# Kernel optimization log

Hardware: AMD Instinct MI355X
Metric: run time of the kernel (lower is better)

The kernel has to match this reference:

```python
import jax, jax.numpy as jnp
import numpy as np


def _rms(x, w=None, eps=1e-6):
    # RMSNorm in fp32 like the torch module, optional elementwise affine.
    x32 = x.astype(jnp.float32)
    r = jax.lax.rsqrt(jnp.mean(x32 * x32, axis=-1, keepdims=True) + eps)
    y = (x32 * r).astype(x.dtype)
    return y * w if w is not None else y


def _rotate_half(x):
    x1, x2 = jnp.split(x, 2, axis=-1)
    return jnp.concatenate([-x2, x1], axis=-1)


def setup_inputs() -> dict:
    key = jax.random.key(0)
    ks = jax.random.split(key, 10)
    B, N, C, H = 16, 1024, 1152, 16
    hd = C // H          # 72
    hid = 3072           # _swiglu_hidden(1152, 4.0)
    grid = 32            # grid**2 == N
    quarter = hd // 4    # 18
    # exact axial RoPE cache (build_axial_rope_cache)
    inv_freq = 1.0 / (10000.0 ** (np.arange(quarter, dtype=np.float32) / quarter))
    pos = np.arange(grid, dtype=np.float32)
    f1 = pos[:, None] * inv_freq[None, :]                               # (grid, quarter)
    fy = np.broadcast_to(f1[:, None, :], (grid, grid, quarter)).reshape(-1, quarter)
    fx = np.broadcast_to(f1[None, :, :], (grid, grid, quarter)).reshape(-1, quarter)

    def cs(f):
        e = np.concatenate([f, f], axis=-1)                             # (N, hd//2)
        return jnp.asarray(np.cos(e))[None, None], jnp.asarray(np.sin(e))[None, None]

    cos_y, sin_y = cs(fy)
    cos_x, sin_x = cs(fx)

    def w(k, shp, scale=0.02):
        return jax.random.normal(k, shp, jnp.float32) * scale

    return {
        "x": jax.random.normal(ks[0], (B, N, C), jnp.float32),
        "temb": jax.random.normal(ks[1], (B, C), jnp.float32),
        "cos_y": cos_y, "sin_y": sin_y, "cos_x": cos_x, "sin_x": sin_x,
        "Wqkv": w(ks[2], (3 * C, C)), "bqkv": jnp.zeros((3 * C,), jnp.float32),
        "Wt": w(ks[3], (3 * C, C)), "bt": jnp.zeros((3 * C,), jnp.float32),
        "Wp": w(ks[4], (C, C)), "bp": jnp.zeros((C,), jnp.float32),
        "qn_w": jnp.ones((hd,), jnp.float32), "kn_w": jnp.ones((hd,), jnp.float32),
        "Wg": w(ks[5], (hid, C)), "bg": jnp.zeros((hid,), jnp.float32),
        "Wu": w(ks[6], (hid, C)), "bu": jnp.zeros((hid,), jnp.float32),
        "Wd": w(ks[7], (C, hid)), "bd": jnp.zeros((C,), jnp.float32),
    }


def reference(x, temb, cos_y, sin_y, cos_x, sin_x, Wqkv, bqkv, Wt, bt, Wp, bp,
              qn_w, kn_w, Wg, bg, Wu, bu, Wd, bd):
    B, N, C = x.shape
    H = 16
    hd = C // H

    # --- TMSA attention branch ---
    xn = _rms(x)                                            # norm1 (no affine)
    qkv = xn @ Wqkv.T + bqkv + (temb @ Wt.T + bt)[:, None, :]
    qkv = qkv.reshape(B, N, 3, H, hd).transpose(2, 0, 3, 1, 4)  # (3,B,H,N,hd)
    q, k, v = qkv[0], qkv[1], qkv[2]
    q = _rms(q, qn_w)
    k = _rms(k, kn_w)

    def rope(t):
        ty, tx = jnp.split(t, 2, axis=-1)
        ty = ty * cos_y + _rotate_half(ty) * sin_y
        tx = tx * cos_x + _rotate_half(tx) * sin_x
        return jnp.concatenate([ty, tx], axis=-1)

    q, k = rope(q), rope(k)

    scores = jnp.einsum('bhnd,bhmd->bhnm', q, k) / jnp.sqrt(jnp.float32(hd))
    attn = jax.nn.softmax(scores, axis=-1)
    o = jnp.einsum('bhnm,bhmd->bhnd', attn, v)
    o = o.transpose(0, 2, 1, 3).reshape(B, N, C)
    x = x + (o @ Wp.T + bp)

    # --- SwiGLU MLP branch ---
    xn2 = _rms(x)                                           # norm2 (no affine)
    h = jax.nn.silu(xn2 @ Wg.T + bg) * (xn2 @ Wu.T + bu)
    x = x + (h @ Wd.T + bd)
    return x
```

## Files before the change

kernel.cpp:

```cpp
#include <hip/hip_runtime.h>
#include <cstdint>
#include <cstddef>

typedef unsigned short u16;
typedef unsigned int u32;
typedef __attribute__((ext_vector_type(8))) short bf16x8s;
typedef __attribute__((ext_vector_type(4))) float f32x4;

__device__ __forceinline__ u16 f2bf(float f){
  union { float f; unsigned u; } v; v.f = f;
  unsigned r = v.u + 0x7FFFu + ((v.u >> 16) & 1u);
  return (u16)(r >> 16);
}
__device__ __forceinline__ float bf2f(u16 h){
  union { unsigned u; float f; } v; v.u = ((unsigned)h) << 16;
  return v.f;
}

__global__ __launch_bounds__(256) void cvt_kernel(const float* __restrict__ in,
                                                  u16* __restrict__ out, int n){
  int i = blockIdx.x*256 + threadIdx.x;
  if (i < n) out[i] = f2bf(in[i]);
}

__global__ __launch_bounds__(256) void cvt_gu_kernel(const float* __restrict__ Wg,
                                                     const float* __restrict__ Wu,
                                                     u16* __restrict__ out){
  size_t i = (size_t)blockIdx.x*256 + threadIdx.x;
  if (i >= (size_t)6144*1152) return;
  int j = (int)(i / 1152), k = (int)(i % 1152);
  int b16 = j >> 4, w = j & 15;
  int src = (b16 >> 1)*16 + w;
  const float* W = (b16 & 1) ? Wu : Wg;
  out[i] = f2bf(W[(size_t)src*1152 + k]);
}

__global__ __launch_bounds__(256) void temb_kernel(const float* __restrict__ temb,
                                                   const float* __restrict__ Wt,
                                                   const float* __restrict__ bt,
                                                   const float* __restrict__ bqkv,
                                                   float* __restrict__ tvec){
  const int col  = blockIdx.x*4 + (threadIdx.x>>6);
  const int lane = threadIdx.x & 63;
  const float* wp = Wt + (size_t)col*1152;
  float w[18];
  #pragma unroll
  for (int j=0;j<18;j++) w[j] = wp[lane + j*64];
  float acc[16];
  #pragma unroll
  for (int b=0;b<16;b++) acc[b] = 0.f;
  #pragma unroll
  for (int j=0;j<18;j++){
    const int k = lane + j*64;
    #pragma unroll
    for (int b=0;b<16;b++) acc[b] += w[j]*temb[b*1152 + k];
  }
  #pragma unroll
  for (int b=0;b<16;b++){
    #pragma unroll
    for (int d=1; d<64; d<<=1) acc[b] += __shfl_xor(acc[b], d);
  }
  if (lane == 0){
    float add = bt[col] + bqkv[col];
    #pragma unroll
    for (int b=0;b<16;b++) tvec[(size_t)b*3456 + col] = acc[b] + add;
  }
}

__global__ __launch_bounds__(256) void rms_kernel(const float* __restrict__ in,
                                                  u16* __restrict__ out, int C){
  int row = blockIdx.x;
  const float* p = in + (size_t)row*C;
  float ss = 0.f;
  for (int c = threadIdx.x; c < C; c += 256){ float v = p[c]; ss += v*v; }
  #pragma unroll
  for (int d=1; d<64; d<<=1) ss += __shfl_xor(ss, d);
  __shared__ float wsum[4];
  if ((threadIdx.x & 63) == 0) wsum[threadIdx.x>>6] = ss;
  __syncthreads();
  float tot = wsum[0]+wsum[1]+wsum[2]+wsum[3];
  float r = rsqrtf(tot/(float)C + 1e-6f);
  u16* o = out + (size_t)row*C;
  for (int c = threadIdx.x; c < C; c += 256) o[c] = f2bf(p[c]*r);
}

template<int MODE>
__global__ __launch_bounds__(512, 4) void gemm_kernel(
    const u16* __restrict__ A, const u16* __restrict__ B,
    int M, int N, int K, int nbx, int segw,
    const float* __restrict__ bias, const float* __restrict__ fextra,
    void* __restrict__ outv, u16* __restrict__ out2, u16* __restrict__ out3)
{
  __shared__ __align__(16) u16 As0[256*32];
  __shared__ __align__(16) u16 As1[256*32];
  __shared__ __align__(16) u16 As2[256*32];
  __shared__ __align__(16) u16 Bs0[128*32];
  __shared__ __align__(16) u16 Bs1[128*32];
  __shared__ __align__(16) u16 Bs2[128*32];
  const int tid  = threadIdx.x;
  const int lane = tid & 63;
  const int wv   = tid >> 6;
  const int wr   = wv >> 1, wc = wv & 1;

  const int nwg  = (int)gridDim.x;
  const int bid  = (int)blockIdx.x;
  const int xcd  = bid & 7;
  const int slot = bid >> 3;
  const int mdep = (nwg >> 3) / nbx;
  const int segsz = mdep * segw;
  const int seg  = slot / segsz;
  const int rem  = slot - seg*segsz;
  const int mi   = rem / segw;
  const int ni   = seg*segw + (rem - mi*segw);
  const long m0 = (long)(xcd*mdep + mi) * 256;
  const long n0 = (long)ni * 128;

  const u16* Ab = A + (size_t)m0*K;
  const u16* Bb = B + (size_t)n0*K;

  const int gsw  = ((lane&3) ^ ((lane>>3)&3)) * 8;
  const int srow = lane >> 2;

  f32x4 acc[4][4];
  #pragma unroll
  for (int i=0;i<4;i++)
    #pragma unroll
    for (int j=0;j<4;j++) acc[i][j] = (f32x4){0.f,0.f,0.f,0.f};

  auto stage = [&](u16* as, u16* bs, int kt){
    __builtin_amdgcn_global_load_lds(
      (const __attribute__((address_space(1))) void*)(Ab + (size_t)(wv*16 + srow)*K + kt + gsw),
      (__attribute__((address_space(3))) void*)(as + wv*512), 16, 0, 0);
    __builtin_amdgcn_global_load_lds(
      (const __attribute__((address_space(1))) void*)(Ab + (size_t)(128 + wv*16 + srow)*K + kt + gsw),
      (__attribute__((address_space(3))) void*)(as + 4096 + wv*512), 16, 0, 0);
    __builtin_amdgcn_global_load_lds(
      (const __attribute__((address_space(1))) void*)(Bb + (size_t)(wv*16 + srow)*K + kt + gsw),
      (__attribute__((address_space(3))) void*)(bs + wv*512), 16, 0, 0);
  };
  auto compute = [&](const u16* as, const u16* bs){
    const int swc = (((lane>>4) ^ ((lane>>1)&3))) * 8;
    const int lc16 = lane & 15;
    bf16x8s af[4], bfr[4];
    #pragma unroll
    for (int i=0;i<4;i++)
      af[i] = *(const bf16x8s*)(as + (wr*64 + i*16 + lc16)*32 + swc);
    #pragma unroll
    for (int j=0;j<4;j++)
      bfr[j] = *(const bf16x8s*)(bs + (wc*64 + j*16 + lc16)*32 + swc);
    #pragma unroll
    for (int i=0;i<4;i++)
      #pragma unroll
      for (int j=0;j<4;j++)
        acc[i][j] = __builtin_amdgcn_mfma_f32_16x16x32_bf16(af[i], bfr[j], acc[i][j], 0,0,0);
  };

  const int NT = K >> 5;
  stage(As0, Bs0, 0);
  stage(As1, Bs1, 32);
  asm volatile("s_waitcnt vmcnt(3)" ::: "memory");
  __builtin_amdgcn_s_barrier();
  __builtin_amdgcn_sched_barrier(0);

  for (int t = 0; t < NT; t += 3){
    if (t+2 < NT) stage(As2, Bs2, (t+2)*32);
    compute(As0, Bs0);
    if (t+2 < NT) asm volatile("s_waitcnt vmcnt(3)" ::: "memory");
    else          asm volatile("s_waitcnt vmcnt(0)" ::: "memory");
    __builtin_amdgcn_s_barrier();
    __builtin_amdgcn_sched_barrier(0);
    if (t+3 < NT) stage(As0, Bs0, (t+3)*32);
    compute(As1, Bs1);
    if (t+3 < NT) asm volatile("s_waitcnt vmcnt(3)" ::: "memory");
    else          asm volatile("s_waitcnt vmcnt(0)" ::: "memory");
    __builtin_amdgcn_s_barrier();
    __builtin_amdgcn_sched_barrier(0);
    if (t+4 < NT) stage(As1, Bs1, (t+4)*32);
    compute(As2, Bs2);
    if (t+4 < NT) asm volatile("s_waitcnt vmcnt(3)" ::: "memory");
    else          asm volatile("s_waitcnt vmcnt(0)" ::: "memory");
    __builtin_amdgcn_s_barrier();
    __builtin_amdgcn_sched_barrier(0);
  }

  const int lr = (lane>>4)*4, lc = lane&15;
  if (MODE==5){
    #pragma unroll
    for (int i=0;i<4;i++){
      #pragma unroll
      for (int jp=0;jp<2;jp++){
        long hcol = (n0>>1) + wc*32 + jp*16 + lc;
        float bgv = bias[hcol], buv = fextra[hcol];
        #pragma unroll
        for (int r=0;r<4;r++){
          long rowg = m0 + wr*64 + i*16 + lr + r;
          float gv = acc[i][2*jp][r] + bgv;
          float uv = acc[i][2*jp+1][r] + buv;
          float hv = (gv/(1.f + __expf(-gv))) * uv;
          ((u16*)outv)[(size_t)rowg*3072 + hcol] = f2bf(hv);
        }
      }
    }
    return;
  }
  #pragma unroll
  for (int i=0;i<4;i++){
    #pragma unroll
    for (int j=0;j<4;j++){
      long colg = n0 + wc*64 + j*16 + lc;
      long rowg0 = m0 + wr*64 + i*16 + lr;
      if (MODE==0){
        int cg = (int)colg;
        int which = cg / 1152;
        int rem2 = cg - which*1152;
        int hh = rem2 / 72, dd = rem2 - hh*72;
        int b = (int)(rowg0 >> 10), n = (int)(rowg0 & 1023);
        size_t bh = (size_t)(b*16 + hh);
        float tadd = fextra[(size_t)b*3456 + colg];
        if (which == 2){
          ushort4 vv;
          vv.x = f2bf(acc[i][j][0] + tadd);
          vv.y = f2bf(acc[i][j][1] + tadd);
          vv.z = f2bf(acc[i][j][2] + tadd);
          vv.w = f2bf(acc[i][j][3] + tadd);
          *(ushort4*)(out3 + (bh*72 + dd)*1024 + n) = vv;
        } else {
          u16* dst = (which==0) ? (u16*)outv : out2;
          #pragma unroll
          for (int r=0;r<4;r++)
            dst[(bh*1024 + (size_t)(n + r))*72 + dd] = f2bf(acc[i][j][r] + tadd);
        }
      } else {
        #pragma unroll
        for (int r=0;r<4;r++){
          long rowg = rowg0 + r;
          float v = acc[i][j][r];
          size_t oi = (size_t)rowg*N + colg;
          v += bias[colg] + fextra[oi];
          ((float*)outv)[oi] = v;
        }
      }
    }
  }
}

__global__ __launch_bounds__(256) void qkrope_kernel(
    u16* __restrict__ Q, u16* __restrict__ K,
    const float* __restrict__ qn_w, const float* __restrict__ kn_w,
    const float* __restrict__ cos_y, const float* __restrict__ sin_y,
    const float* __restrict__ cos_x, const float* __restrict__ sin_x)
{
  const int gw   = blockIdx.x*4 + (threadIdx.x>>6);
  const int lane = threadIdx.x & 63;
  const int n = gw & 1023;
  const int d0 = lane*2;
  const bool act = d0 < 72;
  const float scale = 0.11785113019775793f;

  u16* qp = Q + (size_t)gw*72;
  u16* kp = K + (size_t)gw*72;
  float q0=0,q1=0,k0=0,k1=0,wq0=0,wq1=0,wk0=0,wk1=0;
  if (act){
    q0 = bf2f(qp[d0]); q1 = bf2f(qp[d0+1]);
    k0 = bf2f(kp[d0]); k1 = bf2f(kp[d0+1]);
    wq0 = qn_w[d0]; wq1 = qn_w[d0+1];
    wk0 = kn_w[d0]; wk1 = kn_w[d0+1];
  }
  float ssq = q0*q0 + q1*q1;
  float ssk = k0*k0 + k1*k1;
  #pragma unroll
  for (int d=1; d<64; d<<=1){ ssq += __shfl_xor(ssq,d); ssk += __shfl_xor(ssk,d); }
  const float rq = rsqrtf(ssq*(1.f/72.f) + 1e-6f);
  const float rk = rsqrtf(ssk*(1.f/72.f) + 1e-6f);
  float qn0 = q0*rq*wq0, qn1 = q1*rq*wq1;
  float kn0 = k0*rk*wk0, kn1 = k1*rk*wk1;

  int dh = d0 % 36;
  const bool first = (dh < 18);
  int partner = first ? lane+9 : lane-9;
  if (!act) partner = lane;
  float pq0 = __shfl(qn0, partner), pq1 = __shfl(qn1, partner);
  float pk0 = __shfl(kn0, partner), pk1 = __shfl(kn1, partner);
  if (act){
    const float* cp = (d0 < 36) ? cos_y : cos_x;
    const float* sp = (d0 < 36) ? sin_y : sin_x;
    float c0 = cp[n*36+dh], c1 = cp[n*36+dh+1];
    float s0 = sp[n*36+dh], s1 = sp[n*36+dh+1];
    float sgn = first ? -1.f : 1.f;
    float qo0 = (qn0*c0 + sgn*pq0*s0)*scale, qo1 = (qn1*c1 + sgn*pq1*s1)*scale;
    float ko0 = kn0*c0 + sgn*pk0*s0,         ko1 = kn1*c1 + sgn*pk1*s1;
    *(unsigned*)(qp + d0) = (unsigned)f2bf(qo0) | ((unsigned)f2bf(qo1)<<16);
    *(unsigned*)(kp + d0) = (unsigned)f2bf(ko0) | ((unsigned)f2bf(ko1)<<16);
  }
}

__global__ __launch_bounds__(256, 3) void attn_kernel(
    const u16* __restrict__ Q, const u16* __restrict__ K,
    const u16* __restrict__ Vt, u16* __restrict__ O)
{
  const int tid  = threadIdx.x;
  const int lane = tid & 63;
  const int wv   = tid >> 6;
  const int g = lane >> 4, c = lane & 15;
  const int bid  = blockIdx.x;
  const int head = (bid >> 6) * 8 + (bid & 7);
  const int q0   = ((bid >> 3) & 7) * 128;
  const int b = head >> 4, h = head & 15;

  __shared__ __align__(16) u16 Vlds[80][72];
  __shared__ __align__(16) u16 Plds[8][16][64];

  const bf16x8s zf = {0,0,0,0,0,0,0,0};
  const u16* Kp = K + (size_t)head*1024*72;
  const u16* Qb = Q + ((size_t)head*1024 + q0 + wv*32)*72;
  const char* Vg = (const char*)(Vt + (size_t)head*72*1024);

  bf16x8s qf[2][3];
  #pragma unroll
  for (int s=0;s<2;s++){
    const u16* qrow = Qb + (size_t)(s*16 + c)*72;
    qf[s][0] = *(const bf16x8s*)(qrow + g*8);
    qf[s][1] = *(const bf16x8s*)(qrow + 32 + g*8);
    qf[s][2] = (g==0) ? *(const bf16x8s*)(qrow + 64) : zf;
  }

  f32x4 oacc[2][5];
  float lsum[2] = {0.f, 0.f};
  #pragma unroll
  for (int s=0;s<2;s++)
    #pragma unroll
    for (int c5=0;c5<5;c5++) oacc[s][c5] = (f32x4){0.f,0.f,0.f,0.f};

  char* pb0 = (char*)Plds + (wv*2+0)*2048 + c*128;
  char* pb1 = pb0 + 2048;
  const int swz = (c & 7) << 4;

  int4 vr0, vr1, vr2;
  {
    vr0 = *(const int4*)(Vg + ((tid    )>>3)*2048 + ((tid    )&7)*16);
    vr1 = *(const int4*)(Vg + ((256+tid)>>3)*2048 + ((256+tid)&7)*16);
    if (tid < 64) vr2 = *(const int4*)(Vg + ((512+tid)>>3)*2048 + ((512+tid)&7)*16);
  }
  if (tid < 288) ((u32*)&Vlds[72][0])[tid] = 0u;
  {
    *(int4*)((char*)Vlds + ((tid    )>>3)*144 + ((tid    )&7)*16) = vr0;
    *(int4*)((char*)Vlds + ((256+tid)>>3)*144 + ((256+tid)&7)*16) = vr1;
    if (tid < 64) *(int4*)((char*)Vlds + ((512+tid)>>3)*144 + ((512+tid)&7)*16) = vr2;
  }

  for (int t = 0; t < 16; ++t){
    const int kv0 = t*64;
    __syncthreads();
    if (t < 15){
      const char* vs = Vg + (kv0+64)*2;
      vr0 = *(const int4*)(vs + ((tid    )>>3)*2048 + ((tid    )&7)*16);
      vr1 = *(const int4*)(vs + ((256+tid)>>3)*2048 + ((256+tid)&7)*16);
      if (tid < 64) vr2 = *(const int4*)(vs + ((512+tid)>>3)*2048 + ((512+tid)&7)*16);
    }

    #pragma unroll
    for (int nf=0; nf<4; nf++){
      const u16* krow = Kp + (size_t)(kv0 + nf*16 + c)*72;
      bf16x8s kf0 = *(const bf16x8s*)(krow + g*8);
      bf16x8s kf1 = *(const bf16x8s*)(krow + 32 + g*8);
      bf16x8s kf2 = (g==0) ? *(const bf16x8s*)(krow + 64) : zf;
      #pragma unroll
      for (int s=0;s<2;s++){
        f32x4 sc = (f32x4){0.f,0.f,0.f,0.f};
        sc = __builtin_amdgcn_mfma_f32_16x16x32_bf16(kf0, qf[s][0], sc,0,0,0);
        sc = __builtin_amdgcn_mfma_f32_16x16x32_bf16(kf1, qf[s][1], sc,0,0,0);
        sc = __builtin_amdgcn_mfma_f32_16x16x32_bf16(kf2, qf[s][2], sc,0,0,0);
        float p0 = __expf(sc[0]), p1 = __expf(sc[1]);
        float p2 = __expf(sc[2]), p3 = __expf(sc[3]);
        lsum[s] += (p0+p1) + (p2+p3);
        u32 w0 = (u32)f2bf(p0) | ((u32)f2bf(p1) << 16);
        u32 w1 = (u32)f2bf(p2) | ((u32)f2bf(p3) << 16);
        char* pb = s ? pb1 : pb0;
        int kb = nf*32 + g*8;
        *(u32*)(pb + ( kb      ^ swz)) = w0;
        *(u32*)(pb + ((kb + 4) ^ swz)) = w1;
      }
    }
    asm volatile("" ::: "memory");
    bf16x8s pa[2][2];
    #pragma unroll
    for (int s=0;s<2;s++)
      #pragma unroll
      for (int w2=0;w2<2;w2++)
        pa[s][w2] = *(const bf16x8s*)((s?pb1:pb0) + ((w2*64 + g*16) ^ swz));

    #pragma unroll
    for (int c5=0;c5<5;c5++){
      #pragma unroll
      for (int w2=0;w2<2;w2++){
        bf16x8s vf = *(const bf16x8s*)((const char*)Vlds + (size_t)(c5*16+c)*144 + w2*64 + g*16);
        oacc[0][c5] = __builtin_amdgcn_mfma_f32_16x16x32_bf16(pa[0][w2], vf, oacc[0][c5],0,0,0);
        oacc[1][c5] = __builtin_amdgcn_mfma_f32_16x16x32_bf16(pa[1][w2], vf, oacc[1][c5],0,0,0);
      }
    }

    if (t < 15){
      __syncthreads();
      *(int4*)((char*)Vlds + ((tid    )>>3)*144 + ((tid    )&7)*16) = vr0;
      *(int4*)((char*)Vlds + ((256+tid)>>3)*144 + ((256+tid)&7)*16) = vr1;
      if (tid < 64) *(int4*)((char*)Vlds + ((512+tid)>>3)*144 + ((512+tid)&7)*16) = vr2;
    }
  }

  size_t obase = (size_t)b*1024*1152 + (size_t)h*72;
  #pragma unroll
  for (int s=0;s<2;s++){
    float ls = lsum[s];
    ls += __shfl_xor(ls, 16);
    ls += __shfl_xor(ls, 32);
    float linv[4];
    #pragma unroll
    for (int r=0;r<4;r++) linv[r] = 1.0f / __shfl(ls, 4*g + r);
    #pragma unroll
    for (int c5=0;c5<5;c5++){
      int d = c5*16 + c;
      if (d < 72){
        #pragma unroll
        for (int r=0;r<4;r++){
          int n = q0 + wv*32 + s*16 + 4*g + r;
          O[obase + (size_t)n*1152 + d] = f2bf(oacc[s][c5][r]*linv[r]);
        }
      }
    }
  }
}

extern "C" void kernel_launch(void* const* d_in, const int* in_sizes, int n_in,
                              void* d_out, int out_size, void* d_ws, size_t ws_size,
                              hipStream_t stream) {
  const float* x    = (const float*)d_in[0];
  const float* temb = (const float*)d_in[1];
  const float* cos_y= (const float*)d_in[2];
  const float* sin_y= (const float*)d_in[3];
  const float* cos_x= (const float*)d_in[4];
  const float* sin_x= (const float*)d_in[5];
  const float* Wqkv = (const float*)d_in[6];
  const float* bqkv = (const float*)d_in[7];
  const float* Wt   = (const float*)d_in[8];
  const float* bt   = (const float*)d_in[9];
  const float* Wp   = (const float*)d_in[10];
  const float* bp   = (const float*)d_in[11];
  const float* qn_w = (const float*)d_in[12];
  const float* kn_w = (const float*)d_in[13];
  const float* Wg   = (const float*)d_in[14];
  const float* bg   = (const float*)d_in[15];
  const float* Wu   = (const float*)d_in[16];
  const float* bu   = (const float*)d_in[17];
  const float* Wd   = (const float*)d_in[18];
  const float* bd   = (const float*)d_in[19];

  char* ws = (char*)d_ws;
  size_t off = 0;
  auto alloc = [&](size_t bytes)->void*{
    off = (off + 255) & ~(size_t)255;
    void* p = ws + off; off += bytes; return p;
  };

  u16*   wbuf  = (u16*)alloc((size_t)6144*1152*2);
  float* tvec  = (float*)alloc((size_t)16*3456*4);
  u16*   xn_bf = (u16*)alloc((size_t)16384*1152*2);
  u16*   qt    = (u16*)alloc((size_t)262144*72*2);
  u16*   kt    = (u16*)alloc((size_t)262144*72*2);
  u16*   vt    = (u16*)alloc((size_t)256*72*1024*2);
  if (off > ws_size) return;

  u16*   o_bf   = xn_bf;
  u16*   xn2_bf = xn_bf;
  u16*   gbuf   = qt;
  float* x1     = (float*)d_out;

  rms_kernel<<<16384,256,0,stream>>>(x, xn_bf, 1152);
  temb_kernel<<<864,256,0,stream>>>(temb, Wt, bt, bqkv, tvec);

  cvt_kernel<<<(3456*1152+255)/256,256,0,stream>>>(Wqkv, wbuf, 3456*1152);
  gemm_kernel<0><<<64*27,512,0,stream>>>(
      xn_bf, wbuf, 16384, 3456, 1152, 27, 9, nullptr, tvec, qt, kt, vt);

  qkrope_kernel<<<65536,256,0,stream>>>(qt, kt, qn_w, kn_w, cos_y, sin_y, cos_x, sin_x);

  attn_kernel<<<2048,256,0,stream>>>(qt, kt, vt, o_bf);

  cvt_kernel<<<(1152*1152+255)/256,256,0,stream>>>(Wp, wbuf, 1152*1152);
  gemm_kernel<1><<<64*9,512,0,stream>>>(
      o_bf, wbuf, 16384, 1152, 1152, 9, 9, bp, x, x1, nullptr, nullptr);

  rms_kernel<<<16384,256,0,stream>>>(x1, xn2_bf, 1152);

  cvt_gu_kernel<<<(6144*1152+255)/256,256,0,stream>>>(Wg, Wu, wbuf);
  gemm_kernel<5><<<64*48,512,0,stream>>>(
      xn2_bf, wbuf, 16384, 6144, 1152, 48, 8, bg, bu, gbuf, nullptr, nullptr);

  cvt_kernel<<<(1152*3072+255)/256,256,0,stream>>>(Wd, wbuf, 1152*3072);
  gemm_kernel<4><<<64*9,512,0,stream>>>(
      gbuf, wbuf, 16384, 1152, 3072, 9, 3, bd, x1, (float*)d_out, nullptr, nullptr);
}
```

Before: 1.020 ms.

## Add 256x256-tile gate/up GEMM kernel with K=64 double-buffered pipeline

Replaces the generic 256x128 gemm_kernel<5> path for the fused gate/up projection with a dedicated kernel using 256x256 output tiles, K-step 64, and XOR-swizzled LDS staging. Global-to-LDS loads for the next tiles are interleaved across four sub-phases of each k-tile, and s_setprio is raised around the MFMA bursts. The larger tile raises arithmetic intensity per block and halves the block count. In exchange it needs 128KB of LDS and 128 accumulator registers per thread, which limits occupancy.

Result: no change. 1.004 ms (-1.6%).

```diff
diff --git a/kernel.cpp b/kernel.cpp
--- a/kernel.cpp
+++ b/kernel.cpp
@@ -6,6 +6,9 @@
 typedef unsigned int u32;
 typedef __attribute__((ext_vector_type(8))) short bf16x8s;
 typedef __attribute__((ext_vector_type(4))) float f32x4;
+
+#define ASG __attribute__((address_space(1)))
+#define ASL __attribute__((address_space(3)))
 
 __device__ __forceinline__ u16 f2bf(float f){
   union { float f; unsigned u; } v; v.f = f;
@@ -129,14 +132,14 @@
 
   auto stage = [&](u16* as, u16* bs, int kt){
     __builtin_amdgcn_global_load_lds(
-      (const __attribute__((address_space(1))) void*)(Ab + (size_t)(wv*16 + srow)*K + kt + gsw),
-      (__attribute__((address_space(3))) void*)(as + wv*512), 16, 0, 0);
+      (const ASG void*)(Ab + (size_t)(wv*16 + srow)*K + kt + gsw),
+      (ASL void*)(as + wv*512), 16, 0, 0);
     __builtin_amdgcn_global_load_lds(
-      (const __attribute__((address_space(1))) void*)(Ab + (size_t)(128 + wv*16 + srow)*K + kt + gsw),
-      (__attribute__((address_space(3))) void*)(as + 4096 + wv*512), 16, 0, 0);
+      (const ASG void*)(Ab + (size_t)(128 + wv*16 + srow)*K + kt + gsw),
+      (ASL void*)(as + 4096 + wv*512), 16, 0, 0);
     __builtin_amdgcn_global_load_lds(
-      (const __attribute__((address_space(1))) void*)(Bb + (size_t)(wv*16 + srow)*K + kt + gsw),
-      (__attribute__((address_space(3))) void*)(bs + wv*512), 16, 0, 0);
+      (const ASG void*)(Bb + (size_t)(wv*16 + srow)*K + kt + gsw),
+      (ASL void*)(bs + wv*512), 16, 0, 0);
   };
   auto compute = [&](const u16* as, const u16* bs){
     const int swc = (((lane>>4) ^ ((lane>>1)&3))) * 8;
@@ -184,25 +187,6 @@
   }
 
   const int lr = (lane>>4)*4, lc = lane&15;
-  if (MODE==5){
-    #pragma unroll
-    for (int i=0;i<4;i++){
-      #pragma unroll
-      for (int jp=0;jp<2;jp++){
-        long hcol = (n0>>1) + wc*32 + jp*16 + lc;
-        float bgv = bias[hcol], buv = fextra[hcol];
-        #pragma unroll
-        for (int r=0;r<4;r++){
-          long rowg = m0 + wr*64 + i*16 + lr + r;
-          float gv = acc[i][2*jp][r] + bgv;
-          float uv = acc[i][2*jp+1][r] + buv;
-          float hv = (gv/(1.f + __expf(-gv))) * uv;
-          ((u16*)outv)[(size_t)rowg*3072 + hcol] = f2bf(hv);
-        }
-      }
-    }
-    return;
-  }
   #pragma unroll
   for (int i=0;i<4;i++){
     #pragma unroll
@@ -244,6 +228,140 @@
   }
 }
 
+__global__ __launch_bounds__(512, 2) void gemm_gu8(
+    const u16* __restrict__ A, const u16* __restrict__ B,
+    int K, int nbx, int segw,
+    const float* __restrict__ bg, const float* __restrict__ bu,
+    u16* __restrict__ out)
+{
+  __shared__ __align__(16) u16 As0[256*64];
+  __shared__ __align__(16) u16 Bs0[256*64];
+  __shared__ __align__(16) u16 As1[256*64];
+  __shared__ __align__(16) u16 Bs1[256*64];
+  const int tid  = threadIdx.x;
+  const int lane = tid & 63;
+  const int wv   = tid >> 6;
+  const int wr   = wv >> 2;
+  const int wc   = wv & 3;
+  const int g = lane >> 4, c = lane & 15;
+
+  const int nwg  = (int)gridDim.x;
+  const int bid  = (int)blockIdx.x;
+  const int xcd  = bid & 7;
+  const int slot = bid >> 3;
+  const int mdep = (nwg >> 3) / nbx;
+  const int segsz = mdep * segw;
+  const int seg  = slot / segsz;
+  const int rem  = slot - seg*segsz;
+  const int mi   = rem / segw;
+  const int ni   = seg*segw + (rem - mi*segw);
+  const long m0 = (long)(xcd*mdep + mi) * 256;
+  const long n0 = (long)ni * 256;
+
+  const u16* Ab = A + (size_t)m0*K;
+  const u16* Bb = B + (size_t)n0*K;
+
+  const int srow = tid >> 3;
+  const int q8   = ((tid & 7) ^ (srow & 7)) * 8;
+
+  auto stageTo = [&](u16* dst, const u16* src, int h, int kt){
+    __builtin_amdgcn_global_load_lds(
+      (const ASG void*)(src + (size_t)(h*128 + srow)*K + kt + q8),
+      (ASL void*)(dst + h*8192 + wv*512), 16, 0, 0);
+    __builtin_amdgcn_global_load_lds(
+      (const ASG void*)(src + (size_t)(h*128 + 64 + srow)*K + kt + q8),
+      (ASL void*)(dst + h*8192 + 4096 + wv*512), 16, 0, 0);
+  };
+
+  f32x4 acc[8][4];
+  #pragma unroll
+  for (int i=0;i<8;i++)
+    #pragma unroll
+    for (int j=0;j<4;j++) acc[i][j] = (f32x4){0.f,0.f,0.f,0.f};
+
+  const int sw0 = ((g     ) ^ (c & 7)) * 16;
+  const int sw1 = ((4 + g ) ^ (c & 7)) * 16;
+
+  const int NT = K >> 6;
+
+  stageTo(As0, Ab, 0, 0);  stageTo(As0, Ab, 1, 0);
+  stageTo(Bs0, Bb, 0, 0);  stageTo(Bs0, Bb, 1, 0);
+  stageTo(Bs1, Bb, 0, 64); stageTo(Bs1, Bb, 1, 64);
+  asm volatile("s_waitcnt vmcnt(4)" ::: "memory");
+  __builtin_amdgcn_s_barrier();
+  __builtin_amdgcn_sched_barrier(0);
+
+  auto ktile = [&](const u16* CA, u16* CB, u16* NA, int t){
+    const char* aB = (const char*)CA + wr*16384;
+    const char* bB = (const char*)CB + (wc>>1)*16384;
+    bf16x8s bfr[4][2];
+    #pragma unroll
+    for (int p=0;p<4;p++){
+      const int r0 = (2*p)*16 + c;
+      const int r1 = r0 + 16;
+      bf16x8s a00 = *(const bf16x8s*)(aB + r0*128 + sw0);
+      bf16x8s a01 = *(const bf16x8s*)(aB + r0*128 + sw1);
+      bf16x8s a10 = *(const bf16x8s*)(aB + r1*128 + sw0);
+      bf16x8s a11 = *(const bf16x8s*)(aB + r1*128 + sw1);
+      if (p==0){
+        #pragma unroll
+        for (int j=0;j<4;j++){
+          const int br = (wc&1)*64 + j*16 + c;
+          bfr[j][0] = *(const bf16x8s*)(bB + br*128 + sw0);
+          bfr[j][1] = *(const bf16x8s*)(bB + br*128 + sw1);
+        }
+        if (t+1 < NT) stageTo(NA, Ab, 0, (t+1)*64);
+      } else if (p==1){
+        if (t+1 < NT) stageTo(NA, Ab, 1, (t+1)*64);
+      } else if (p==2){
+        if (t+2 < NT) stageTo(CB, Bb, 0, (t+2)*64);
+      } else {
+        if (t+2 < NT) stageTo(CB, Bb, 1, (t+2)*64);
+      }
+      __builtin_amdgcn_s_barrier();
+      asm volatile("s_waitcnt lgkmcnt(0)" ::: "memory");
+      __builtin_amdgcn_sched_barrier(0);
+      __builtin_amdgcn_s_setprio(1);
+      #pragma unroll
+      for (int j=0;j<4;j++){
+        acc[2*p  ][j] = __builtin_amdgcn_mfma_f32_16x16x32_bf16(a00, bfr[j][0], acc[2*p  ][j],0,0,0);
+        acc[2*p  ][j] = __builtin_amdgcn_mfma_f32_16x16x32_bf16(a01, bfr[j][1], acc[2*p  ][j],0,0,0);
+        acc[2*p+1][j] = __builtin_amdgcn_mfma_f32_16x16x32_bf16(a10, bfr[j][0], acc[2*p+1][j],0,0,0);
+        acc[2*p+1][j] = __builtin_amdgcn_mfma_f32_16x16x32_bf16(a11, bfr[j][1], acc[2*p+1][j],0,0,0);
+      }
+      __builtin_amdgcn_s_setprio(0);
+      if (p==3){
+        if (t+2 < NT) asm volatile("s_waitcnt vmcnt(4)" ::: "memory");
+        else          asm volatile("s_waitcnt vmcnt(0)" ::: "memory");
+      }
+      __builtin_amdgcn_s_barrier();
+      __builtin_amdgcn_sched_barrier(0);
+    }
+  };
+
+  for (int tp = 0; tp < NT; tp += 2){
+    ktile(As0, Bs0, As1, tp);
+    ktile(As1, Bs1, As0, tp+1);
+  }
+
+  #pragma unroll
+  for (int i=0;i<8;i++){
+    #pragma unroll
+    for (int jp=0;jp<2;jp++){
+      long hcol = (n0>>1) + wc*32 + jp*16 + c;
+      float bgv = bg[hcol], buv = bu[hcol];
+      #pragma unroll
+      for (int r=0;r<4;r++){
+        long rowg = m0 + wr*128 + i*16 + g*4 + r;
+        float gv = acc[i][2*jp  ][r] + bgv;
+        float uv = acc[i][2*jp+1][r] + buv;
+        float hv = (gv/(1.f + __expf(-gv))) * uv;
+        out[(size_t)rowg*3072 + hcol] = f2bf(hv);
+      }
+    }
+  }
+}
+
 __global__ __launch_bounds__(256) void qkrope_kernel(
     u16* __restrict__ Q, u16* __restrict__ K,
     const float* __restrict__ qn_w, const float* __restrict__ kn_w,
@@ -492,8 +610,8 @@
   rms_kernel<<<16384,256,0,stream>>>(x1, xn2_bf, 1152);
 
   cvt_gu_kernel<<<(6144*1152+255)/256,256,0,stream>>>(Wg, Wu, wbuf);
-  gemm_kernel<5><<<64*48,512,0,stream>>>(
-      xn2_bf, wbuf, 16384, 6144, 1152, 48, 8, bg, bu, gbuf, nullptr, nullptr);
+  gemm_gu8<<<1536,512,0,stream>>>(
+      xn2_bf, wbuf, 1152, 24, 4, bg, bu, gbuf);
 
   cvt_kernel<<<(1152*3072+255)/256,256,0,stream>>>(Wd, wbuf, 1152*3072);
   gemm_kernel<4><<<64*9,512,0,stream>>>(
```
